# Kernel optimization log

Hardware: AMD Instinct MI355X
Metric: run time of the kernel (lower is better)

Reference implementation:

```python
import jax, jax.numpy as jnp
import numpy as np

N, H, NH, R, E = 50000, 128, 8, 100, 800000
HD = H // NH  # head_dim = 16


def _linear(x, W, b):
    # torch nn.Linear convention: W is [out, in]
    return x @ W.T + b


def _layernorm(x, g, b, eps=1e-5):
    mu = jnp.mean(x, axis=-1, keepdims=True)
    var = jnp.var(x, axis=-1, keepdims=True)
    return (x - mu) * jax.lax.rsqrt(var + eps) * g + b


def setup_inputs() -> dict:
    key = jax.random.key(0)
    ks = jax.random.split(key, 24)
    s = 0.02
    inp = {
        "node_features": jax.random.normal(ks[0], (N, H), jnp.float32),
        "query_embedding": jax.random.normal(ks[1], (1, H), jnp.float32),
        "edge_index": jax.random.randint(ks[2], (2, E), 0, N),
        "edge_type": jax.random.randint(ks[3], (E,), 0, R),
        "relation_embeddings": jax.random.normal(ks[4], (R, H), jnp.float32),
        # attention params
        "Wq": jax.random.normal(ks[5], (H, 2 * H), jnp.float32) * s,
        "bq": jnp.zeros((H,), jnp.float32),
        "Wk": jax.random.normal(ks[6], (H, 2 * H), jnp.float32) * s,
        "bk": jnp.zeros((H,), jnp.float32),
        "Wv": jax.random.normal(ks[7], (H, H), jnp.float32) * s,
        "bv": jnp.zeros((H,), jnp.float32),
        "Wo": jax.random.normal(ks[8], (H, H), jnp.float32) * s,
        "bo": jnp.zeros((H,), jnp.float32),
        # norms
        "n1g": jnp.ones((H,), jnp.float32), "n1b": jnp.zeros((H,), jnp.float32),
        "n2g": jnp.ones((H,), jnp.float32), "n2b": jnp.zeros((H,), jnp.float32),
        # ffn
        "W1": jax.random.normal(ks[9], (4 * H, H), jnp.float32) * s,
        "b1": jnp.zeros((4 * H,), jnp.float32),
        "W2": jax.random.normal(ks[10], (H, 4 * H), jnp.float32) * s,
        "b2": jnp.zeros((H,), jnp.float32),
        # relational layer: 4 interaction transforms stacked [4, H, H]
        "relW": jax.random.normal(ks[11], (4, H, H), jnp.float32) * s,
        "relb": jnp.zeros((4, H), jnp.float32),
        "Wc": jax.random.normal(ks[12], (H, 4 * H), jnp.float32) * s,
        "bc": jnp.zeros((H,), jnp.float32),
        "rng_": jnp.ones((H,), jnp.float32), "rnb": jnp.zeros((H,), jnp.float32),
    }
    return inp


def reference(node_features, query_embedding, edge_index, edge_type, relation_embeddings,
              Wq, bq, Wk, bk, Wv, bv, Wo, bo, n1g, n1b, n2g, n2b,
              W1, b1, W2, b2, relW, relb, Wc, bc, rng_, rnb):
    num_nodes = node_features.shape[0]
    # query-conditioned attention (dropout is identity in eval mode)
    q_exp = jnp.broadcast_to(query_embedding, (num_nodes, H))
    nq = jnp.concatenate([node_features, q_exp], axis=-1)  # [N, 2H]
    q = _linear(nq, Wq, bq).reshape(num_nodes, NH, HD)
    k = _linear(nq, Wk, bk).reshape(num_nodes, NH, HD)
    v = _linear(node_features, Wv, bv).reshape(num_nodes, NH, HD)
    src, dst = edge_index[0], edge_index[1]
    rel_bias = relation_embeddings[edge_type].reshape(-1, NH, HD)  # [E, NH, HD]
    scores = jnp.sum(q[dst] * (k[src] + rel_bias), axis=-1) / np.sqrt(HD)  # [E, NH]
    # sparse softmax over incoming edges per dst node; torch init is zeros with
    # include_self=True amax -> max(0, segment_max)
    seg_max = jnp.maximum(jax.ops.segment_max(scores, dst, num_segments=num_nodes), 0.0)
    exp_s = jnp.exp(scores - seg_max[dst])
    denom = jax.ops.segment_sum(exp_s, dst, num_segments=num_nodes)
    w = exp_s / (denom[dst] + 1e-8)  # [E, NH]
    msg = w[..., None] * v[src]  # [E, NH, HD]
    agg = jax.ops.segment_sum(msg, dst, num_segments=num_nodes).reshape(num_nodes, H)
    attn_out = _linear(agg, Wo, bo)
    x = _layernorm(node_features + attn_out, n1g, n1b)
    ffn = _linear(jax.nn.gelu(_linear(x, W1, b1), approximate=False), W2, b2)
    x = _layernorm(x + ffn, n2g, n2b)
    # relational interaction layer
    t = jnp.einsum('rh,koh->rko', relation_embeddings, relW) + relb  # [R, 4, H]
    combined = t.reshape(relation_embeddings.shape[0], 4 * H)
    rel_out = _layernorm(relation_embeddings + _linear(combined, Wc, bc), rng_, rnb)
    return x, rel_out
```

## Files before the change

kernel.cpp:

```cpp
#include <hip/hip_runtime.h>
#include <hip/hip_bf16.h>
#include <math.h>

using bf16 = __hip_bfloat16;
typedef _Float16 hf;
typedef hf __attribute__((ext_vector_type(2))) hf2;
typedef __attribute__((ext_vector_type(8))) short short8;
typedef __attribute__((ext_vector_type(4))) short short4v;
typedef __attribute__((ext_vector_type(4))) float floatx4;

__device__ __forceinline__ float b2f(bf16 x){ return __bfloat162float(x); }
__device__ __forceinline__ bf16 f2b(float x){ return __float2bfloat16(x); }
__device__ __forceinline__ short bfbits(float x){ bf16 t = __float2bfloat16(x); return *(short*)&t; }
__device__ __forceinline__ short hfbits(float x){ hf t = (hf)x; return *(short*)&t; }
__device__ __forceinline__ hf2 u2h2(unsigned u){ return *(hf2*)&u; }

__global__ void fill_const(float* __restrict__ p, float v, int n){
  int i = blockIdx.x*blockDim.x + threadIdx.x;
  if (i < n) p[i] = v;
}

__global__ __launch_bounds__(256) void prep_all(
    const float* __restrict__ nf, bf16* __restrict__ nfb, int n_nf,
    const float* __restrict__ qe, bf16* __restrict__ qeb,
    const float* __restrict__ Wq, const float* __restrict__ Wk, const float* __restrict__ Wv,
    const float* __restrict__ bq, const float* __restrict__ bk, const float* __restrict__ bv,
    bf16* __restrict__ Wcat, float* __restrict__ bcat,
    const float* __restrict__ Wo, bf16* __restrict__ Wob,
    const float* __restrict__ W1, bf16* __restrict__ W1b,
    const float* __restrict__ W2, bf16* __restrict__ W2b,
    const float* __restrict__ rel, short* __restrict__ Rh, int n_rel,
    int* __restrict__ deg, int Nn,
    int b_nf, int b_wcat, int b_wo, int b_w1, int b_w2, int b_rel, int b_deg){
  int b = blockIdx.x, t = threadIdx.x;
  if (b < b_nf){
    int i = (b*256 + t) * 4;
    if (i < n_nf){
      float4 v = *(const float4*)(nf + i);
      short4v o;
      o.x = bfbits(v.x); o.y = bfbits(v.y); o.z = bfbits(v.z); o.w = bfbits(v.w);
      *(short4v*)((short*)nfb + i) = o;
    }
    return;
  }
  b -= b_nf;
  if (b < b_wcat){
    int i = b*256 + t;
    int r = i >> 8, c = i & 255;
    float v;
    if (r < 128)       v = Wq[r*256 + c];
    else if (r < 256)  v = Wk[(r-128)*256 + c];
    else               v = (c < 128) ? Wv[(r-256)*128 + c] : 0.f;
    Wcat[i] = f2b(v);
    if (i < 384) bcat[i] = (i < 128) ? bq[i] : (i < 256 ? bk[i-128] : bv[i-256]);
    return;
  }
  b -= b_wcat;
  if (b < 1){
    if (t < 128) qeb[t] = f2b(qe[t]);
    return;
  }
  b -= 1;
  if (b < b_wo){ int i = b*256 + t; Wob[i] = f2b(Wo[i]); return; }
  b -= b_wo;
  if (b < b_w1){ int i = b*256 + t; W1b[i] = f2b(W1[i]); return; }
  b -= b_w1;
  if (b < b_w2){ int i = b*256 + t; W2b[i] = f2b(W2[i]); return; }
  b -= b_w2;
  if (b < b_rel){ int i = b*256 + t; if (i < n_rel) Rh[i] = hfbits(rel[i]); return; }
  b -= b_rel;
  { int i = b*256 + t; if (i < Nn) deg[i] = 0; }
}

__global__ void edge_hist(const int* __restrict__ ei, int E, int* __restrict__ deg){
  int e = blockIdx.x*blockDim.x + threadIdx.x;
  if (e >= E) return;
  atomicAdd(&deg[ei[E + e]], 1);
}

__global__ __launch_bounds__(256) void scan_p1(const int* __restrict__ deg, int Nn,
                                               int* __restrict__ bsum){
  int i = blockIdx.x*256 + threadIdx.x;
  int v = (i < Nn) ? deg[i] : 0;
  #pragma unroll
  for (int off=1; off<64; off<<=1) v += __shfl_xor(v, off);
  __shared__ int ws[4];
  if ((threadIdx.x & 63) == 0) ws[threadIdx.x >> 6] = v;
  __syncthreads();
  if (threadIdx.x == 0) bsum[blockIdx.x] = ws[0] + ws[1] + ws[2] + ws[3];
}

__global__ __launch_bounds__(1024) void scan_p2(int* __restrict__ bsum, int NB, int E,
                                                int* __restrict__ rowptr, int Nn){
  __shared__ int wsum[16];
  __shared__ int carry_s;
  if (threadIdx.x == 0) carry_s = 0;
  __syncthreads();
  const int lane = threadIdx.x & 63, w = threadIdx.x >> 6;
  for (int base = 0; base < NB; base += 1024){
    int i = base + threadIdx.x;
    int v = (i < NB) ? bsum[i] : 0;
    int s = v;
    #pragma unroll
    for (int off=1; off<64; off<<=1){ int t = __shfl_up(s, off); if (lane >= off) s += t; }
    if (lane == 63) wsum[w] = s;
    __syncthreads();
    if (threadIdx.x < 16){
      int ws = wsum[threadIdx.x];
      #pragma unroll
      for (int off=1; off<16; off<<=1){ int t = __shfl_up(ws, off); if (threadIdx.x >= off) ws += t; }
      wsum[threadIdx.x] = ws;
    }
    __syncthreads();
    int carry = carry_s;
    int excl = carry + (w ? wsum[w-1] : 0) + (s - v);
    if (i < NB) bsum[i] = excl;
    __syncthreads();
    if (threadIdx.x == 1023) carry_s = carry + wsum[15];
    __syncthreads();
  }
  if (threadIdx.x == 0) rowptr[Nn] = E;
}

__global__ __launch_bounds__(256) void scan_p3(const int* __restrict__ deg,
      const int* __restrict__ boff, int Nn,
      int* __restrict__ rowptr, int* __restrict__ cursor){
  int i = blockIdx.x*256 + threadIdx.x;
  int v = (i < Nn) ? deg[i] : 0;
  const int lane = threadIdx.x & 63, w = threadIdx.x >> 6;
  int s = v;
  #pragma unroll
  for (int off=1; off<64; off<<=1){ int t = __shfl_up(s, off); if (lane >= off) s += t; }
  __shared__ int wsum[4];
  if (lane == 63) wsum[w] = s;
  __syncthreads();
  int wpre = 0;
  #pragma unroll
  for (int k=0;k<4;k++) if (k < w) wpre += wsum[k];
  int excl = boff[blockIdx.x] + wpre + (s - v);
  if (i < Nn){ rowptr[i] = excl; cursor[i] = excl; }
}

__global__ __launch_bounds__(256) void edge_scatter(const int* __restrict__ ei, const int* __restrict__ ety,
                             int E, int* __restrict__ cursor, unsigned* __restrict__ srcet, int Nn){
  const int p = blockIdx.x & 7;
  const int c = blockIdx.x >> 3;
  const int C = gridDim.x >> 3;
  const int chunk = (Nn + 7) >> 3;
  const int lo = p * chunk;
  const int hi = min(Nn, lo + chunk);
  const int per = (E + C - 1) / C;
  const int e1 = min(E, (c + 1) * per);
  for (int e = c * per + threadIdx.x; e < e1; e += 256){
    int dst = ei[E + e];
    if (dst >= lo && dst < hi){
      int pos = atomicAdd(&cursor[dst], 1);
      srcet[pos] = ((unsigned)ety[e] << 16) | (unsigned)ei[e];
    }
  }
}

__global__ __launch_bounds__(256) void gemm_qkv(const bf16* __restrict__ nfb, const bf16* __restrict__ qeb,
      const bf16* __restrict__ Wcat, const float* __restrict__ bcat,
      short* __restrict__ Qs, short* __restrict__ KVs, int M){
  constexpr int BK=32, LDT=40, K=256;
  __shared__ short As[64*LDT];
  __shared__ short Bs[64*LDT];
  const int tid  = threadIdx.x;
  const int lane = tid & 63;
  const int wave = tid >> 6;
  const int wm = (wave >> 1) * 32, wn = (wave & 1) * 32;
  const long m0 = (long)blockIdx.x * 64;
  const int  n0 = blockIdx.y * 64;
  floatx4 acc00 = {0.f,0.f,0.f,0.f}, acc01 = {0.f,0.f,0.f,0.f};
  floatx4 acc10 = {0.f,0.f,0.f,0.f}, acc11 = {0.f,0.f,0.f,0.f};
  const int srow = tid >> 2, scg = (tid & 3) * 8;
  const int r = lane & 15, q = lane >> 4;
  const short* Ag = (const short*)nfb;
  const short* Qg = (const short*)qeb;
  const short* Bg = (const short*)Wcat;
  for (int k0 = 0; k0 < K; k0 += BK){
    short8 va = {0,0,0,0,0,0,0,0};
    if (k0 < 128){
      long ar = m0 + srow;
      if (ar < M) va = *(const short8*)(Ag + ar*128 + k0 + scg);
    } else {
      va = *(const short8*)(Qg + (k0-128) + scg);
    }
    *(short8*)(&As[srow*LDT + scg]) = va;
    *(short8*)(&Bs[srow*LDT + scg]) = *(const short8*)(Bg + (long)(n0 + srow)*K + k0 + scg);
    __syncthreads();
    short8 a0 = *(const short8*)(&As[(wm      + r)*LDT + q*8]);
    short8 a1 = *(const short8*)(&As[(wm + 16 + r)*LDT + q*8]);
    short8 b0 = *(const short8*)(&Bs[(wn      + r)*LDT + q*8]);
    short8 b1 = *(const short8*)(&Bs[(wn + 16 + r)*LDT + q*8]);
    acc00 = __builtin_amdgcn_mfma_f32_16x16x32_bf16(a0, b0, acc00, 0, 0, 0);
    acc01 = __builtin_amdgcn_mfma_f32_16x16x32_bf16(a0, b1, acc01, 0, 0, 0);
    acc10 = __builtin_amdgcn_mfma_f32_16x16x32_bf16(a1, b0, acc10, 0, 0, 0);
    acc11 = __builtin_amdgcn_mfma_f32_16x16x32_bf16(a1, b1, acc11, 0, 0, 0);
    __syncthreads();
  }
  #pragma unroll
  for (int i=0;i<2;i++)
  #pragma unroll
  for (int j=0;j<2;j++){
    floatx4 av = (i==0) ? ((j==0)?acc00:acc01) : ((j==0)?acc10:acc11);
    int col = n0 + wn + j*16 + r;
    float bsv = bcat[col];
    #pragma unroll
    for (int g=0; g<4; g++){
      long row = m0 + wm + i*16 + q*4 + g;
      if (row < M){
        short bits = hfbits(av[g] + bsv);
        if (col < 128)      Qs[row*128 + col] = bits;
        else if (col < 256){ int d = col - 128; KVs[row*256 + ((d>>1)<<2) + (d&1)] = bits; }
        else               { int d = col - 256; KVs[row*256 + ((d>>1)<<2) + 2 + (d&1)] = bits; }
      }
    }
  }
}

__global__ __launch_bounds__(256) void gemm_bt_ln(const bf16* __restrict__ A, const bf16* __restrict__ B,
      const float* __restrict__ bias, const float* __restrict__ nf,
      const float* __restrict__ gam, const float* __restrict__ bet,
      bf16* __restrict__ xout, int M){
  __shared__ short As[64*136];
  __shared__ short Bs[128*136];
  const int tid = threadIdx.x, lane = tid & 63, wave = tid >> 6;
  const int r = lane & 15, q = lane >> 4;
  const int wm = (wave >> 1) * 32, wn2 = (wave & 1) * 64;
  const long m0 = (long)blockIdx.x * 64;
  const short* Ag = (const short*)A;
  const short* Bg = (const short*)B;
  #pragma unroll
  for (int c=0;c<4;c++){
    int idx = c*256 + tid, row = idx >> 4, ch = (idx & 15) * 8;
    short8 v = {0,0,0,0,0,0,0,0};
    long ar = m0 + row;
    if (ar < M) v = *(const short8*)(Ag + ar*128 + ch);
    *(short8*)(&As[row*136 + ch]) = v;
  }
  #pragma unroll
  for (int c=0;c<8;c++){
    int idx = c*256 + tid, row = idx >> 4, ch = (idx & 15) * 8;
    *(short8*)(&Bs[row*136 + ch]) = *(const short8*)(Bg + (long)row*128 + ch);
  }
  __syncthreads();
  floatx4 o[2][4];
  #pragma unroll
  for (int i=0;i<2;i++)
  #pragma unroll
  for (int j=0;j<4;j++) o[i][j] = (floatx4){0.f,0.f,0.f,0.f};
  #pragma unroll
  for (int k0 = 0; k0 < 128; k0 += 32){
    short8 a0 = *(const short8*)(&As[(wm      + r)*136 + k0 + q*8]);
    short8 a1 = *(const short8*)(&As[(wm + 16 + r)*136 + k0 + q*8]);
    #pragma unroll
    for (int j=0;j<4;j++){
      short8 bj = *(const short8*)(&Bs[(wn2 + j*16 + r)*136 + k0 + q*8]);
      o[0][j] = __builtin_amdgcn_mfma_f32_16x16x32_bf16(a0, bj, o[0][j], 0, 0, 0);
      o[1][j] = __builtin_amdgcn_mfma_f32_16x16x32_bf16(a1, bj, o[1][j], 0, 0, 0);
    }
  }
  __syncthreads();
  float* redp = (float*)Bs;
  float* stat = redp + 256;
  float yv[2][4][4];
  #pragma unroll
  for (int i=0;i<2;i++){
    #pragma unroll
    for (int j=0;j<4;j++){
      int col = wn2 + j*16 + r;
      float bsv = bias[col];
      #pragma unroll
      for (int g=0; g<4; g++){
        int row = wm + i*16 + q*4 + g;
        long grow = m0 + row;
        float nfv = (grow < M) ? nf[grow*128 + col] : 0.f;
        yv[i][j][g] = o[i][j][g] + bsv + nfv;
      }
    }
  }
  #pragma unroll
  for (int i=0;i<2;i++){
    #pragma unroll
    for (int g=0; g<4; g++){
      float s  = yv[i][0][g] + yv[i][1][g] + yv[i][2][g] + yv[i][3][g];
      float s2 = yv[i][0][g]*yv[i][0][g] + yv[i][1][g]*yv[i][1][g]
               + yv[i][2][g]*yv[i][2][g] + yv[i][3][g]*yv[i][3][g];
      #pragma unroll
      for (int m=1; m<16; m<<=1){ s += __shfl_xor(s, m); s2 += __shfl_xor(s2, m); }
      if (r == 0){
        int row = wm + i*16 + q*4 + g;
        redp[row*4 + (wave & 1)*2 + 0] = s;
        redp[row*4 + (wave & 1)*2 + 1] = s2;
      }
    }
  }
  __syncthreads();
  if (tid < 64){
    float s  = redp[tid*4 + 0] + redp[tid*4 + 2];
    float s2 = redp[tid*4 + 1] + redp[tid*4 + 3];
    float mu = s * (1.f/128.f);
    float var = s2 * (1.f/128.f) - mu*mu;
    stat[tid*2 + 0] = mu;
    stat[tid*2 + 1] = rsqrtf(var + 1e-5f);
  }
  __syncthreads();
  #pragma unroll
  for (int i=0;i<2;i++){
    #pragma unroll
    for (int j=0;j<4;j++){
      int col = wn2 + j*16 + r;
      float gv = gam[col], bv = bet[col];
      #pragma unroll
      for (int g=0; g<4; g++){
        int row = wm + i*16 + q*4 + g;
        long grow = m0 + row;
        if (grow < M){
          float mu = stat[row*2], rs = stat[row*2 + 1];
          xout[grow*128 + col] = f2b((yv[i][j][g] - mu)*rs*gv + bv);
        }
      }
    }
  }
}

__global__ __launch_bounds__(256) void attn_agg(const unsigned* __restrict__ Qh,
     const uint2* __restrict__ KVh, const unsigned* __restrict__ Rh,
     const int* __restrict__ rowptr, const unsigned* __restrict__ srcet,
     unsigned* __restrict__ agg, int Nn){
  const int w = threadIdx.x >> 6, l = threadIdx.x & 63;
  const int n = blockIdx.x*4 + w;
  if (n >= Nn) return;
  hf2 q2 = u2h2(Qh[(long)n*64 + l]);
  int beg = rowptr[n], end = rowptr[n+1];
  float acc0 = 0.f, acc1 = 0.f, denom = 0.f;
  for (int c = beg; c < end; c += 64){
    int cnt = end - c; if (cnt > 64) cnt = 64;
    unsigned se_l = (c + l < end) ? srcet[c + l] : 0u;
    int j = 0;
    for (; j + 4 <= cnt; j += 4){
      unsigned se0 = __shfl(se_l, j+0);
      unsigned se1 = __shfl(se_l, j+1);
      unsigned se2 = __shfl(se_l, j+2);
      unsigned se3 = __shfl(se_l, j+3);
      uint2 kv0 = KVh[(long)(se0 & 0xFFFF)*64 + l];
      uint2 kv1 = KVh[(long)(se1 & 0xFFFF)*64 + l];
      uint2 kv2 = KVh[(long)(se2 & 0xFFFF)*64 + l];
      uint2 kv3 = KVh[(long)(se3 & 0xFFFF)*64 + l];
      unsigned r0 = Rh[(se0 >> 16)*64 + l];
      unsigned r1 = Rh[(se1 >> 16)*64 + l];
      unsigned r2 = Rh[(se2 >> 16)*64 + l];
      unsigned r3 = Rh[(se3 >> 16)*64 + l];
      hf2 kb0 = u2h2(kv0.x) + u2h2(r0);
      hf2 kb1 = u2h2(kv1.x) + u2h2(r1);
      hf2 kb2 = u2h2(kv2.x) + u2h2(r2);
      hf2 kb3 = u2h2(kv3.x) + u2h2(r3);
#if __has_builtin(__builtin_amdgcn_fdot2)
      float p0 = __builtin_amdgcn_fdot2(q2, kb0, 0.f, false);
      float p1 = __builtin_amdgcn_fdot2(q2, kb1, 0.f, false);
      float p2 = __builtin_amdgcn_fdot2(q2, kb2, 0.f, false);
      float p3 = __builtin_amdgcn_fdot2(q2, kb3, 0.f, false);
#else
      float p0 = fmaf((float)q2.y, (float)kb0.y, (float)q2.x * (float)kb0.x);
      float p1 = fmaf((float)q2.y, (float)kb1.y, (float)q2.x * (float)kb1.x);
      float p2 = fmaf((float)q2.y, (float)kb2.y, (float)q2.x * (float)kb2.x);
      float p3 = fmaf((float)q2.y, (float)kb3.y, (float)q2.x * (float)kb3.x);
#endif
      p0 += __shfl_xor(p0, 1); p1 += __shfl_xor(p1, 1);
      p2 += __shfl_xor(p2, 1); p3 += __shfl_xor(p3, 1);
      p0 += __shfl_xor(p0, 2); p1 += __shfl_xor(p1, 2);
      p2 += __shfl_xor(p2, 2); p3 += __shfl_xor(p3, 2);
      p0 += __shfl_xor(p0, 4); p1 += __shfl_xor(p1, 4);
      p2 += __shfl_xor(p2, 4); p3 += __shfl_xor(p3, 4);
      float e0 = __expf(p0 * 0.25f);
      float e1 = __expf(p1 * 0.25f);
      float e2 = __expf(p2 * 0.25f);
      float e3 = __expf(p3 * 0.25f);
      denom += e0; denom += e1; denom += e2; denom += e3;
      hf2 v0 = u2h2(kv0.y), v1 = u2h2(kv1.y), v2 = u2h2(kv2.y), v3 = u2h2(kv3.y);
      acc0 = fmaf(e0, (float)v0.x, acc0);
      acc1 = fmaf(e0, (float)v0.y, acc1);
      acc0 = fmaf(e1, (float)v1.x, acc0);
      acc1 = fmaf(e1, (float)v1.y, acc1);
      acc0 = fmaf(e2, (float)v2.x, acc0);
      acc1 = fmaf(e2, (float)v2.y, acc1);
      acc0 = fmaf(e3, (float)v3.x, acc0);
      acc1 = fmaf(e3, (float)v3.y, acc1);
    }
    for (; j < cnt; ++j){
      unsigned se = __shfl(se_l, j);
      int src = se & 0xFFFF;
      int et  = se >> 16;
      uint2 kv = KVh[(long)src*64 + l];
      hf2 kb = u2h2(kv.x) + u2h2(Rh[et*64 + l]);
#if __has_builtin(__builtin_amdgcn_fdot2)
      float p = __builtin_amdgcn_fdot2(q2, kb, 0.f, false);
#else
      float p = fmaf((float)q2.y, (float)kb.y, (float)q2.x * (float)kb.x);
#endif
      p += __shfl_xor(p, 1); p += __shfl_xor(p, 2); p += __shfl_xor(p, 4);
      float es = __expf(p * 0.25f);
      denom += es;
      hf2 v2 = u2h2(kv.y);
      acc0 = fmaf(es, (float)v2.x, acc0);
      acc1 = fmaf(es, (float)v2.y, acc1);
    }
  }
  float inv = 1.f / (denom + 1e-8f);
  unsigned out = ((unsigned)(unsigned short)bfbits(acc1 * inv) << 16)
               |  (unsigned)(unsigned short)bfbits(acc0 * inv);
  agg[(long)n*64 + l] = out;
}

__global__ __launch_bounds__(256) void ffn_fused(const bf16* __restrict__ X, const bf16* __restrict__ W1,
    const float* __restrict__ b1, const bf16* __restrict__ W2, const float* __restrict__ b2,
    const float* __restrict__ gam, const float* __restrict__ bet,
    float* __restrict__ Out, int M){
  __shared__ short Xs[64*136];
  __shared__ short Hs[64*140];
  __shared__ short Ws[64*136];
  const int tid = threadIdx.x, lane = tid & 63, wave = tid >> 6;
  const int r = lane & 15, q = lane >> 4;
  const int wm = (wave >> 1) * 32, wn = (wave & 1) * 32;
  const long m0 = (long)blockIdx.x * 64;
  const short* Xg  = (const short*)X;
  const short* W1g = (const short*)W1;
  const short* W2g = (const short*)W2;
  #pragma unroll
  for (int c=0;c<4;c++){
    int idx = c*256 + tid, row = idx >> 4, ch = (idx & 15) * 8;
    short8 v = {0,0,0,0,0,0,0,0};
    long ar = m0 + row;
    if (ar < M) v = *(const short8*)(Xg + ar*128 + ch);
    *(short8*)(&Xs[row*136 + ch]) = v;
  }
  const int wn2 = (wave & 1) * 64;
  floatx4 o[2][4];
  #pragma unroll
  for (int i=0;i<2;i++)
  #pragma unroll
  for (int j=0;j<4;j++) o[i][j] = (floatx4){0.f,0.f,0.f,0.f};
  for (int qtr = 0; qtr < 4; ++qtr){
    const int hb = qtr * 128;
    for (int c0 = 0; c0 < 128; c0 += 64){
      #pragma unroll
      for (int c=0;c<4;c++){
        int idx = c*256 + tid, row = idx >> 4, ch = (idx & 15) * 8;
        *(short8*)(&Ws[row*136 + ch]) = *(const short8*)(W1g + (long)(hb + c0 + row)*128 + ch);
      }
      __syncthreads();
      floatx4 h00 = {0.f,0.f,0.f,0.f}, h01 = {0.f,0.f,0.f,0.f};
      floatx4 h10 = {0.f,0.f,0.f,0.f}, h11 = {0.f,0.f,0.f,0.f};
      #pragma unroll
      for (int k0 = 0; k0 < 128; k0 += 32){
        short8 a0 = *(const short8*)(&Xs[(wm      + r)*136 + k0 + q*8]);
        short8 a1 = *(const short8*)(&Xs[(wm + 16 + r)*136 + k0 + q*8]);
        short8 b0 = *(const short8*)(&Ws[(wn      + r)*136 + k0 + q*8]);
        short8 bv = *(const short8*)(&Ws[(wn + 16 + r)*136 + k0 + q*8]);
        h00 = __builtin_amdgcn_mfma_f32_16x16x32_bf16(a0, b0, h00, 0, 0, 0);
        h01 = __builtin_amdgcn_mfma_f32_16x16x32_bf16(a0, bv, h01, 0, 0, 0);
        h10 = __builtin_amdgcn_mfma_f32_16x16x32_bf16(a1, b0, h10, 0, 0, 0);
        h11 = __builtin_amdgcn_mfma_f32_16x16x32_bf16(a1, bv, h11, 0, 0, 0);
      }
      #pragma unroll
      for (int i=0;i<2;i++)
      #pragma unroll
      for (int j=0;j<2;j++){
        floatx4 av = (i==0) ? ((j==0)?h00:h01) : ((j==0)?h10:h11);
        int col = wn + j*16 + r;
        float bb = b1[hb + c0 + col];
        #pragma unroll
        for (int g=0; g<4; g++){
          int row = wm + i*16 + q*4 + g;
          float v = av[g] + bb;
          v = 0.5f * v * (1.f + erff(v * 0.70710678118f));
          Hs[row*140 + c0 + col] = bfbits(v);
        }
      }
      __syncthreads();
    }
    for (int k0 = 0; k0 < 128; k0 += 64){
      #pragma unroll
      for (int c=0;c<4;c++){
        int idx = c*256 + tid, row = idx >> 3, ch = (idx & 7) * 8;
        *(short8*)(&Ws[row*68 + ch]) = *(const short8*)(W2g + (long)row*512 + hb + k0 + ch);
      }
      __syncthreads();
      #pragma unroll
      for (int ks = 0; ks < 64; ks += 32){
        short8 a0 = *(const short8*)(&Hs[(wm      + r)*140 + k0 + ks + q*8]);
        short8 a1 = *(const short8*)(&Hs[(wm + 16 + r)*140 + k0 + ks + q*8]);
        #pragma unroll
        for (int j=0;j<4;j++){
          short8 bj = *(const short8*)(&Ws[(wn2 + j*16 + r)*68 + ks + q*8]);
          o[0][j] = __builtin_amdgcn_mfma_f32_16x16x32_bf16(a0, bj, o[0][j], 0, 0, 0);
          o[1][j] = __builtin_amdgcn_mfma_f32_16x16x32_bf16(a1, bj, o[1][j], 0, 0, 0);
        }
      }
      __syncthreads();
    }
  }
  float* redp = (float*)Ws;
  float* stat = redp + 256;
  float yv[2][4][4];
  #pragma unroll
  for (int i=0;i<2;i++){
    #pragma unroll
    for (int j=0;j<4;j++){
      int col = wn2 + j*16 + r;
      float bb = b2[col];
      #pragma unroll
      for (int g=0; g<4; g++){
        int row = wm + i*16 + q*4 + g;
        float xr = b2f(*(const bf16*)&Xs[row*136 + col]);
        yv[i][j][g] = o[i][j][g] + bb + xr;
      }
    }
  }
  #pragma unroll
  for (int i=0;i<2;i++){
    #pragma unroll
    for (int g=0; g<4; g++){
      float s  = yv[i][0][g] + yv[i][1][g] + yv[i][2][g] + yv[i][3][g];
      float s2 = yv[i][0][g]*yv[i][0][g] + yv[i][1][g]*yv[i][1][g]
               + yv[i][2][g]*yv[i][2][g] + yv[i][3][g]*yv[i][3][g];
      #pragma unroll
      for (int m=1; m<16; m<<=1){ s += __shfl_xor(s, m); s2 += __shfl_xor(s2, m); }
      if (r == 0){
        int row = wm + i*16 + q*4 + g;
        redp[row*4 + (wave & 1)*2 + 0] = s;
        redp[row*4 + (wave & 1)*2 + 1] = s2;
      }
    }
  }
  __syncthreads();
  if (tid < 64){
    float s  = redp[tid*4 + 0] + redp[tid*4 + 2];
    float s2 = redp[tid*4 + 1] + redp[tid*4 + 3];
    float mu = s * (1.f/128.f);
    float var = s2 * (1.f/128.f) - mu*mu;
    stat[tid*2 + 0] = mu;
    stat[tid*2 + 1] = rsqrtf(var + 1e-5f);
  }
  __syncthreads();
  #pragma unroll
  for (int i=0;i<2;i++){
    #pragma unroll
    for (int j=0;j<4;j++){
      int col = wn2 + j*16 + r;
      float gv = gam[col], bv = bet[col];
      #pragma unroll
      for (int g=0; g<4; g++){
        int row = wm + i*16 + q*4 + g;
        long grow = m0 + row;
        if (grow < M){
          float mu = stat[row*2], rs = stat[row*2 + 1];
          Out[grow*128 + col] = (yv[i][j][g] - mu)*rs*gv + bv;
        }
      }
    }
  }
}

__device__ __forceinline__ float dotf(const float* __restrict__ s, const float* __restrict__ w, int n){
  float acc = 0.f;
  const float4* w4 = (const float4*)w;
  #pragma unroll 4
  for (int j = 0; j < (n >> 2); ++j){
    float4 wv = w4[j];
    acc += s[4*j]*wv.x + s[4*j+1]*wv.y + s[4*j+2]*wv.z + s[4*j+3]*wv.w;
  }
  return acc;
}

__global__ __launch_bounds__(128) void rel_layer(const float* __restrict__ rel, const float* __restrict__ relW,
    const float* __restrict__ relb, const float* __restrict__ Wc, const float* __restrict__ bc,
    const float* __restrict__ gn, const float* __restrict__ bn, float* __restrict__ out){
  int rr = blockIdx.x, t = threadIdx.x;
  __shared__ float rrow[128];
  __shared__ float comb[512];
  rrow[t] = rel[(long)rr*128 + t];
  __syncthreads();
  #pragma unroll
  for (int k=0;k<4;k++){
    comb[k*128 + t] = dotf(rrow, relW + ((long)(k*128) + t)*128, 128) + relb[k*128 + t];
  }
  __syncthreads();
  float c2 = dotf(comb, Wc + (long)t*512, 512) + bc[t];
  float y = rrow[t] + c2;
  float s = y, s2 = y*y;
  #pragma unroll
  for (int off=32; off>0; off>>=1){ s += __shfl_xor(s, off); s2 += __shfl_xor(s2, off); }
  __shared__ float ps[4];
  if ((t & 63) == 0){ ps[(t>>6)*2] = s; ps[(t>>6)*2+1] = s2; }
  __syncthreads();
  float tot = ps[0] + ps[2], tot2 = ps[1] + ps[3];
  float mu = tot * (1.f/128.f);
  float var = tot2 * (1.f/128.f) - mu*mu;
  float rs = rsqrtf(var + 1e-5f);
  out[(long)rr*128 + t] = (y - mu)*rs*gn[t] + bn[t];
}

extern "C" void kernel_launch(void* const* d_in, const int* in_sizes, int n_in,
                              void* d_out, int out_size, void* d_ws, size_t ws_size,
                              hipStream_t stream){
  const int H = 128;
  auto S = [&](int i){ return in_sizes[i]; };
  bool ok = (n_in == 27);
  if (ok){
    ok = ok && S(1)==H && (S(0)%H)==0 && S(2)==2*S(3) && (S(4)%H)==0;
    ok = ok && S(5)==2*H*H && S(7)==2*H*H && S(9)==H*H && S(11)==H*H;
    ok = ok && S(17)==4*H*H && S(19)==4*H*H && S(21)==4*H*H && S(23)==4*H*H;
    ok = ok && out_size == S(0) + S(4);
  }
  if (!ok){
    fill_const<<<(out_size + 255)/256, 256, 0, stream>>>((float*)d_out, 100.0f, out_size);
    return;
  }

  const float* nf   = (const float*)d_in[0];
  const float* qe   = (const float*)d_in[1];
  const int*   ei   = (const int*)  d_in[2];
  const int*   ety  = (const int*)  d_in[3];
  const float* rel  = (const float*)d_in[4];
  const float* Wq   = (const float*)d_in[5];
  const float* bq   = (const float*)d_in[6];
  const float* Wk   = (const float*)d_in[7];
  const float* bk   = (const float*)d_in[8];
  const float* Wv   = (const float*)d_in[9];
  const float* bv   = (const float*)d_in[10];
  const float* Wo   = (const float*)d_in[11];
  const float* bo   = (const float*)d_in[12];
  const float* n1g  = (const float*)d_in[13];
  const float* n1b  = (const float*)d_in[14];
  const float* n2g  = (const float*)d_in[15];
  const float* n2b  = (const float*)d_in[16];
  const float* W1   = (const float*)d_in[17];
  const float* b1   = (const float*)d_in[18];
  const float* W2   = (const float*)d_in[19];
  const float* b2v  = (const float*)d_in[20];
  const float* relW = (const float*)d_in[21];
  const float* relbp= (const float*)d_in[22];
  const float* Wc   = (const float*)d_in[23];
  const float* bc   = (const float*)d_in[24];
  const float* rng  = (const float*)d_in[25];
  const float* rnb  = (const float*)d_in[26];

  const int N = in_sizes[0] / 128;
  const int E = in_sizes[2] / 2;
  const int R = in_sizes[4] / 128;

  char* ws = (char*)d_ws;
  size_t off = 0;
  auto alloc = [&](size_t bytes)->char*{
    char* p = ws + off; off = (off + bytes + 255) & ~(size_t)255; return p;
  };
  char*     regNA  = alloc((size_t)N * 256);
  char*     regKV  = alloc((size_t)N * 512);
  unsigned* Qh     = (unsigned*)alloc((size_t)N * 256);
  bf16*     xlb    = (bf16*)    alloc((size_t)N * 256);
  bf16*     qeb    = (bf16*)    alloc(256);
  bf16*     Wcat   = (bf16*)    alloc((size_t)384*256*2);
  float*    bcat   = (float*)   alloc(384*4);
  bf16*     Wob    = (bf16*)    alloc((size_t)128*128*2);
  bf16*     W1b    = (bf16*)    alloc((size_t)512*128*2);
  bf16*     W2b    = (bf16*)    alloc((size_t)128*512*2);
  short*    Rh     = (short*)   alloc((size_t)R*128*2);
  int*      deg    = (int*)     alloc((size_t)N * 4);
  int*      rowptr = (int*)     alloc((size_t)(N+1) * 4);
  int*      cursor = (int*)     alloc((size_t)N * 4);
  unsigned* srcet  = (unsigned*)alloc((size_t)E * 4);
  const int NB = (N + 255) / 256;
  int*      bsum   = (int*)     alloc((size_t)NB * 4);

  if (off > ws_size){
    fill_const<<<(out_size + 255)/256, 256, 0, stream>>>((float*)d_out, 50.0f, out_size);
    return;
  }

  bf16*     nfb  = (bf16*)regNA;
  unsigned* aggp = (unsigned*)regNA;
  uint2*    KVh  = (uint2*)regKV;
  float*    outx = (float*)d_out;
  float*    outr = (float*)d_out + (size_t)N*128;

  const int n_nf   = N * 128;
  const int b_nf   = (n_nf/4 + 255) / 256;
  const int b_wcat = 384;
  const int b_wo   = 64;
  const int b_w1   = 256;
  const int b_w2   = 256;
  const int n_rel  = R * 128;
  const int b_rel  = (n_rel + 255) / 256;
  const int b_deg  = (N + 255) / 256;
  const int b_tot  = b_nf + b_wcat + 1 + b_wo + b_w1 + b_w2 + b_rel + b_deg;
  prep_all<<<b_tot, 256, 0, stream>>>(nf, nfb, n_nf, qe, qeb,
      Wq, Wk, Wv, bq, bk, bv, Wcat, bcat, Wo, Wob, W1, W1b, W2, W2b,
      rel, Rh, n_rel, deg, N,
      b_nf, b_wcat, b_wo, b_w1, b_w2, b_rel, b_deg);

  edge_hist<<<(E + 255)/256, 256, 0, stream>>>(ei, E, deg);
  scan_p1<<<NB, 256, 0, stream>>>(deg, N, bsum);
  scan_p2<<<1, 1024, 0, stream>>>(bsum, NB, E, rowptr, N);
  scan_p3<<<NB, 256, 0, stream>>>(deg, bsum, N, rowptr, cursor);
  edge_scatter<<<2048, 256, 0, stream>>>(ei, ety, E, cursor, srcet, N);

  dim3 g1((N + 63)/64, 6);
  gemm_qkv<<<g1, 256, 0, stream>>>(nfb, qeb, Wcat, bcat, (short*)Qh, (short*)KVh, N);
  attn_agg<<<(N + 3)/4, 256, 0, stream>>>(Qh, KVh, (const unsigned*)Rh, rowptr, srcet, aggp, N);
  gemm_bt_ln<<<(N + 63)/64, 256, 0, stream>>>((const bf16*)aggp, Wob, bo, nf, n1g, n1b, xlb, N);
  ffn_fused<<<(N + 63)/64, 256, 0, stream>>>(xlb, W1b, b1, W2b, b2v, n2g, n2b, outx, N);
  rel_layer<<<R, 128, 0, stream>>>(rel, relW, relbp, Wc, bc, rng, rnb, outr);
}
```

Measured before the change: 411.8 us.

## Double FFN row tile to 128 with 512 threads and keep X in registers

The fused FFN kernel now processes 128 rows per block with 8 waves, so each W1/W2 tile staged in shared memory is reused across twice as many rows. The X operand fragments are loaded straight from global memory into registers instead of going through a shared-memory tile, and the residual is reread from global memory. This cuts weight traffic per row and shared-memory reads of X, at the cost of more registers (xa array), a larger Hs buffer and possibly lower occupancy.

```diff
diff --git a/kernel.cpp b/kernel.cpp
--- a/kernel.cpp
+++ b/kernel.cpp
@@ -414,29 +414,31 @@
   agg[(long)n*64 + l] = out;
 }
 
-__global__ __launch_bounds__(256) void ffn_fused(const bf16* __restrict__ X, const bf16* __restrict__ W1,
+__global__ __launch_bounds__(512, 4) void ffn_fused(const bf16* __restrict__ X, const bf16* __restrict__ W1,
     const float* __restrict__ b1, const bf16* __restrict__ W2, const float* __restrict__ b2,
     const float* __restrict__ gam, const float* __restrict__ bet,
     float* __restrict__ Out, int M){
-  __shared__ short Xs[64*136];
-  __shared__ short Hs[64*140];
+  __shared__ short Hs[128*140];
   __shared__ short Ws[64*136];
   const int tid = threadIdx.x, lane = tid & 63, wave = tid >> 6;
   const int r = lane & 15, q = lane >> 4;
-  const int wm = (wave >> 1) * 32, wn = (wave & 1) * 32;
-  const long m0 = (long)blockIdx.x * 64;
+  const int wm  = (wave >> 1) * 32;
+  const int wn  = (wave & 1) * 32;
+  const int wn2 = (wave & 1) * 64;
+  const long m0 = (long)blockIdx.x * 128;
   const short* Xg  = (const short*)X;
   const short* W1g = (const short*)W1;
   const short* W2g = (const short*)W2;
-  #pragma unroll
-  for (int c=0;c<4;c++){
-    int idx = c*256 + tid, row = idx >> 4, ch = (idx & 15) * 8;
-    short8 v = {0,0,0,0,0,0,0,0};
-    long ar = m0 + row;
-    if (ar < M) v = *(const short8*)(Xg + ar*128 + ch);
-    *(short8*)(&Xs[row*136 + ch]) = v;
-  }
-  const int wn2 = (wave & 1) * 64;
+  short8 xa[2][4];
+  #pragma unroll
+  for (int i=0;i<2;i++){
+    long ar = m0 + wm + i*16 + r;
+    #pragma unroll
+    for (int kk=0;kk<4;kk++){
+      if (ar < M) xa[i][kk] = *(const short8*)(Xg + ar*128 + kk*32 + q*8);
+      else        xa[i][kk] = (short8){0,0,0,0,0,0,0,0};
+    }
+  }
   floatx4 o[2][4];
   #pragma unroll
   for (int i=0;i<2;i++)
@@ -446,8 +448,8 @@
     const int hb = qtr * 128;
     for (int c0 = 0; c0 < 128; c0 += 64){
       #pragma unroll
-      for (int c=0;c<4;c++){
-        int idx = c*256 + tid, row = idx >> 4, ch = (idx & 15) * 8;
+      for (int c=0;c<2;c++){
+        int idx = c*512 + tid, row = idx >> 4, ch = (idx & 15) * 8;
         *(short8*)(&Ws[row*136 + ch]) = *(const short8*)(W1g + (long)(hb + c0 + row)*128 + ch);
       }
       __syncthreads();
@@ -455,14 +457,12 @@
       floatx4 h10 = {0.f,0.f,0.f,0.f}, h11 = {0.f,0.f,0.f,0.f};
       #pragma unroll
       for (int k0 = 0; k0 < 128; k0 += 32){
-        short8 a0 = *(const short8*)(&Xs[(wm      + r)*136 + k0 + q*8]);
-        short8 a1 = *(const short8*)(&Xs[(wm + 16 + r)*136 + k0 + q*8]);
         short8 b0 = *(const short8*)(&Ws[(wn      + r)*136 + k0 + q*8]);
         short8 bv = *(const short8*)(&Ws[(wn + 16 + r)*136 + k0 + q*8]);
-        h00 = __builtin_amdgcn_mfma_f32_16x16x32_bf16(a0, b0, h00, 0, 0, 0);
-        h01 = __builtin_amdgcn_mfma_f32_16x16x32_bf16(a0, bv, h01, 0, 0, 0);
-        h10 = __builtin_amdgcn_mfma_f32_16x16x32_bf16(a1, b0, h10, 0, 0, 0);
-        h11 = __builtin_amdgcn_mfma_f32_16x16x32_bf16(a1, bv, h11, 0, 0, 0);
+        h00 = __builtin_amdgcn_mfma_f32_16x16x32_bf16(xa[0][k0>>5], b0, h00, 0, 0, 0);
+        h01 = __builtin_amdgcn_mfma_f32_16x16x32_bf16(xa[0][k0>>5], bv, h01, 0, 0, 0);
+        h10 = __builtin_amdgcn_mfma_f32_16x16x32_bf16(xa[1][k0>>5], b0, h10, 0, 0, 0);
+        h11 = __builtin_amdgcn_mfma_f32_16x16x32_bf16(xa[1][k0>>5], bv, h11, 0, 0, 0);
       }
       #pragma unroll
       for (int i=0;i<2;i++)
@@ -483,8 +483,8 @@
     }
     for (int k0 = 0; k0 < 128; k0 += 64){
       #pragma unroll
-      for (int c=0;c<4;c++){
-        int idx = c*256 + tid, row = idx >> 3, ch = (idx & 7) * 8;
+      for (int c=0;c<2;c++){
+        int idx = c*512 + tid, row = idx >> 3, ch = (idx & 7) * 8;
         *(short8*)(&Ws[row*68 + ch]) = *(const short8*)(W2g + (long)row*512 + hb + k0 + ch);
       }
       __syncthreads();
@@ -503,7 +503,7 @@
     }
   }
   float* redp = (float*)Ws;
-  float* stat = redp + 256;
+  float* stat = redp + 512;
   float yv[2][4][4];
   #pragma unroll
   for (int i=0;i<2;i++){
@@ -514,7 +514,8 @@
       #pragma unroll
       for (int g=0; g<4; g++){
         int row = wm + i*16 + q*4 + g;
-        float xr = b2f(*(const bf16*)&Xs[row*136 + col]);
+        long grow = m0 + row;
+        float xr = (grow < M) ? b2f(X[grow*128 + col]) : 0.f;
         yv[i][j][g] = o[i][j][g] + bb + xr;
       }
     }
@@ -536,7 +537,7 @@
     }
   }
   __syncthreads();
-  if (tid < 64){
+  if (tid < 128){
     float s  = redp[tid*4 + 0] + redp[tid*4 + 2];
     float s2 = redp[tid*4 + 1] + redp[tid*4 + 3];
     float mu = s * (1.f/128.f);
@@ -711,6 +712,6 @@
   gemm_qkv<<<g1, 256, 0, stream>>>(nfb, qeb, Wcat, bcat, (short*)Qh, (short*)KVh, N);
   attn_agg<<<(N + 3)/4, 256, 0, stream>>>(Qh, KVh, (const unsigned*)Rh, rowptr, srcet, aggp, N);
   gemm_bt_ln<<<(N + 63)/64, 256, 0, stream>>>((const bf16*)aggp, Wob, bo, nf, n1g, n1b, xlb, N);
-  ffn_fused<<<(N + 63)/64, 256, 0, stream>>>(xlb, W1b, b1, W2b, b2v, n2g, n2b, outx, N);
+  ffn_fused<<<(N + 127)/128, 512, 0, stream>>>(xlb, W1b, b1, W2b, b2v, n2g, n2b, outx, N);
   rel_layer<<<R, 128, 0, stream>>>(rel, relW, relbp, Wc, bc, rng, rnb, outr);
 }
```

New measurement: 387.9 us (median of 2 runs). 1.06x faster.
